# Performance work log

Hardware: AMD Instinct MI355X
Metric: run time of the kernel (lower is better)

## Reference

```python
import jax, jax.numpy as jnp
import numpy as np

N = 100000
E = 1600000
D = 128
EIG = 32
NUM_MOTIFS = 64
EPS = 1e-8  # torch cosine_similarity eps


def setup_inputs() -> dict:
    key = jax.random.key(0)
    ks = jax.random.split(key, 12)
    return {
        "q": jax.random.normal(ks[0], (N, D), jnp.float32),
        "k": jax.random.normal(ks[1], (N, D), jnp.float32),
        "v": jax.random.normal(ks[2], (N, D), jnp.float32),
        "eigs": jax.random.normal(ks[3], (N, EIG), jnp.float32),
        "motif_adj_vals": jax.random.uniform(ks[4], (E,), jnp.float32),
        "lambda0": jax.random.normal(ks[5], (1,), jnp.float32) * 0.1,
        "gamma": jax.random.normal(ks[6], (1,), jnp.float32) * 0.1,
        "motif_emb_w": jax.random.uniform(ks[7], (NUM_MOTIFS, 1), jnp.float32),
        "row": jax.random.randint(ks[8], (E,), 0, N, jnp.int32),
        "col": jax.random.randint(ks[9], (E,), 0, N, jnp.int32),
        "motif_ids": jax.random.randint(ks[10], (N,), 0, NUM_MOTIFS, jnp.int32),
    }


def _sparse_softmax(vals, row, n):
    # softmax of per-edge values grouped by destination/row index
    m = jax.ops.segment_max(vals, row, num_segments=n)
    e = jnp.exp(vals - m[row])
    z = jax.ops.segment_sum(e, row, num_segments=n)
    return e / z[row]


def reference(q, k, v, eigs, motif_adj_vals, lambda0, gamma, motif_emb_w,
              row, col, motif_ids):
    sqrt_dim = 1.0 / jnp.sqrt(jnp.asarray(q.shape[1], q.dtype))
    # edge-wise q.k dot product, scaled
    x = jnp.sum(q[row] * k[col], axis=-1) * sqrt_dim          # [E]
    # eig branch (args.model contains 'eig'); note original does NOT scale by sqrt_eig
    y = jnp.sum(eigs[row] * eigs[col], axis=-1)               # [E]
    s0 = x + jnp.exp(lambda0[0]) * y
    # motif branch: embedding lookup + cosine similarity along the edge dim (dim=0)
    me = motif_emb_w[motif_ids][:, 0]                          # [N]
    a, b = me[row], me[col]                                    # [E]
    sim = jnp.sum(a * b) / (jnp.maximum(jnp.linalg.norm(a), EPS)
                            * jnp.maximum(jnp.linalg.norm(b), EPS))
    s1 = motif_adj_vals * gamma[0] * sim                       # [E]
    n = q.shape[0]
    attn = 0.5 * (_sparse_softmax(s0, row, n) + _sparse_softmax(s1, row, n))
    # sparse-dense matmul: out[r] = sum_e attn_e * v[col_e]
    return jax.ops.segment_sum(attn[:, None] * v[col], row, num_segments=n)
```

## Files before the change

### kernel.cpp

```cpp
#include <hip/hip_runtime.h>
#include <math.h>

#define N_NODES 100000
#define N_EDGES 1600000
#define DIM 128
#define EIGD 32
#define CS_EPS 1e-8f

#define B1 1024
#define CHUNK 1563
#define NB 391

static const size_t OFF_REC    = 0;
static const size_t OFF_SW     = 0;
static const size_t OFF_RSTAT  = 6400000;
static const size_t OFF_SE     = 12800000;
static const size_t OFF_GH     = 12800000;
static const size_t OFF_BSTART = 25600000;
static const size_t OFF_BTOT   = 25601600;
static const size_t OFF_GPART  = 25603200;
static const size_t OFF_OFFS   = 25619584;
static const size_t OFF_SCAL   = 26019600;
static const size_t OFF_KB     = 26019616;
static const size_t OFF_VB     = 51619616;
static const size_t OFF_EB     = 77219616;

__device__ __forceinline__ unsigned short f2bf(float f) {
    unsigned u = __float_as_uint(f);
    unsigned r = (u + 0x7fffu + ((u >> 16) & 1u)) >> 16;
    return (unsigned short)r;
}
__device__ __forceinline__ float blo(unsigned w) { return __uint_as_float(w << 16); }
__device__ __forceinline__ float bhi(unsigned w) { return __uint_as_float(w & 0xffff0000u); }

#define K4C 3200000
#define E4C 800000

__global__ void __launch_bounds__(256) ka_cvt(
        const float* __restrict__ k, const float* __restrict__ v,
        const float* __restrict__ eigs,
        ushort* __restrict__ kb, ushort* __restrict__ vb,
        ushort* __restrict__ eb) {
    int i = blockIdx.x * blockDim.x + threadIdx.x;
    const float* src; ushort* dst; int j;
    if (i < K4C)            { src = k;    dst = kb; j = i; }
    else if (i < 2 * K4C)   { src = v;    dst = vb; j = i - K4C; }
    else if (i < 2*K4C+E4C) { src = eigs; dst = eb; j = i - 2 * K4C; }
    else return;
    float4 f = ((const float4*)src)[j];
    ushort4 o;
    o.x = f2bf(f.x); o.y = f2bf(f.y); o.z = f2bf(f.z); o.w = f2bf(f.w);
    ((ushort4*)dst)[j] = o;
}

__global__ void __launch_bounds__(256) kb_hist(
        const int* __restrict__ row, const int* __restrict__ col,
        const float* __restrict__ motif_w, const int* __restrict__ motif_ids,
        int* __restrict__ gh, float4* __restrict__ gpart) {
    __shared__ int hist[NB];
    __shared__ float wlds[64];
    __shared__ float red[3][4];
    const int t = threadIdx.x, b = blockIdx.x;
    for (int i = t; i < NB; i += 256) hist[i] = 0;
    if (t < 64) wlds[t] = motif_w[t];
    __syncthreads();

    const int e0 = b * CHUNK, e1 = min(N_EDGES, e0 + CHUNK);
    float sab = 0.f, saa = 0.f, sbb = 0.f;
    for (int e = e0 + t; e < e1; e += 256) {
        int r = row[e], c = col[e];
        atomicAdd(&hist[r >> 8], 1);
        float mr = wlds[motif_ids[r]], mc = wlds[motif_ids[c]];
        sab += mr * mc; saa += mr * mr; sbb += mc * mc;
    }
#pragma unroll
    for (int off = 32; off >= 1; off >>= 1) {
        sab += __shfl_xor(sab, off);
        saa += __shfl_xor(saa, off);
        sbb += __shfl_xor(sbb, off);
    }
    int lane = t & 63, wid = t >> 6;
    if (lane == 0) { red[0][wid] = sab; red[1][wid] = saa; red[2][wid] = sbb; }
    __syncthreads();
    if (t == 0) {
        float a = 0.f, bb = 0.f, cc = 0.f;
#pragma unroll
        for (int i = 0; i < 4; i++) { a += red[0][i]; bb += red[1][i]; cc += red[2][i]; }
        gpart[b] = make_float4(a, bb, cc, 0.f);
    }
    __syncthreads();
    for (int i = t; i < NB; i += 256) gh[b * NB + i] = hist[i];
}

__global__ void __launch_bounds__(256) ks_scanA(
        int* __restrict__ gh, int* __restrict__ btot) {
    const int colb = blockIdx.x;
    const int t = threadIdx.x;
    int v0 = gh[(t * 4 + 0) * NB + colb];
    int v1 = gh[(t * 4 + 1) * NB + colb];
    int v2 = gh[(t * 4 + 2) * NB + colb];
    int v3 = gh[(t * 4 + 3) * NB + colb];
    int tot4 = v0 + v1 + v2 + v3;
    __shared__ int sc[256];
    sc[t] = tot4;
    __syncthreads();
    for (int off = 1; off < 256; off <<= 1) {
        int w = (t >= off) ? sc[t - off] : 0;
        __syncthreads();
        sc[t] += w;
        __syncthreads();
    }
    int excl = sc[t] - tot4;
    gh[(t * 4 + 0) * NB + colb] = excl;
    gh[(t * 4 + 1) * NB + colb] = excl + v0;
    gh[(t * 4 + 2) * NB + colb] = excl + v0 + v1;
    gh[(t * 4 + 3) * NB + colb] = excl + v0 + v1 + v2;
    if (t == 255) btot[colb] = excl + tot4;
}

__global__ void __launch_bounds__(512) ks_scanB(
        const int* __restrict__ btot, int* __restrict__ bstart,
        const float4* __restrict__ gpart, const float* __restrict__ gamma,
        float* __restrict__ scal, int* __restrict__ offs) {
    const int t = threadIdx.x;
    __shared__ int tot[512];
    int my = (t < NB) ? btot[t] : 0;
    tot[t] = my;
    __syncthreads();
    for (int off = 1; off < 512; off <<= 1) {
        int v = (t >= off) ? tot[t - off] : 0;
        __syncthreads();
        tot[t] += v;
        __syncthreads();
    }
    if (t < NB) bstart[t] = tot[t] - my;
    if (t == NB - 1) {
        bstart[NB] = tot[t];
        offs[N_NODES] = tot[t];
    }

    float4 g0 = gpart[t];
    float4 g1 = gpart[t + 512];
    float sab = g0.x + g1.x, saa = g0.y + g1.y, sbb = g0.z + g1.z;
#pragma unroll
    for (int off = 32; off >= 1; off >>= 1) {
        sab += __shfl_xor(sab, off);
        saa += __shfl_xor(saa, off);
        sbb += __shfl_xor(sbb, off);
    }
    __shared__ float red[3][8];
    int lane = t & 63, wid = t >> 6;
    if (lane == 0) { red[0][wid] = sab; red[1][wid] = saa; red[2][wid] = sbb; }
    __syncthreads();
    if (t == 0) {
        float a = 0.f, bb = 0.f, cc = 0.f;
#pragma unroll
        for (int i = 0; i < 8; i++) { a += red[0][i]; bb += red[1][i]; cc += red[2][i]; }
        float na = sqrtf(bb); if (na < CS_EPS) na = CS_EPS;
        float nb2 = sqrtf(cc); if (nb2 < CS_EPS) nb2 = CS_EPS;
        scal[0] = gamma[0] * (a / (na * nb2));
    }
}

__global__ void __launch_bounds__(256) kd_coarse(
        const int* __restrict__ row, const int* __restrict__ col,
        const float* __restrict__ adj, const int* __restrict__ gh,
        const int* __restrict__ bstart, int2* __restrict__ rec) {
    __shared__ int cur[NB];
    const int t = threadIdx.x, b = blockIdx.x;
    for (int i = t; i < NB; i += 256) cur[i] = bstart[i] + gh[b * NB + i];
    __syncthreads();
    const int e0 = b * CHUNK, e1 = min(N_EDGES, e0 + CHUNK);
    for (int e = e0 + t; e < e1; e += 256) {
        int r = row[e];
        int pos = atomicAdd(&cur[r >> 8], 1);
        rec[pos] = make_int2(col[e] | ((r & 255) << 17), __float_as_int(adj[e]));
    }
}

__global__ void __launch_bounds__(256) kf_fine(
        const int2* __restrict__ rec, const int* __restrict__ bstart,
        int* __restrict__ offs, float2* __restrict__ se) {
    __shared__ int hist[256], sc[256], cur[256];
    const int t = threadIdx.x, b = blockIdx.x;
    hist[t] = 0;
    __syncthreads();
    const int s = bstart[b], e1 = bstart[b + 1];
    for (int i = s + t; i < e1; i += 256) {
        int rl = (rec[i].x >> 17) & 255;
        atomicAdd(&hist[rl], 1);
    }
    __syncthreads();
    int v = hist[t];
    sc[t] = v;
    __syncthreads();
    for (int off = 1; off < 256; off <<= 1) {
        int w = (t >= off) ? sc[t - off] : 0;
        __syncthreads();
        sc[t] += w;
        __syncthreads();
    }
    int excl = sc[t] - v;
    int rowg = b * 256 + t;
    if (rowg < N_NODES) offs[rowg] = s + excl;
    cur[t] = s + excl;
    __syncthreads();
    for (int i = s + t; i < e1; i += 256) {
        int2 rc = rec[i];
        int rl = (rc.x >> 17) & 255;
        int pos = atomicAdd(&cur[rl], 1);
        se[pos] = make_float2(__int_as_float(rc.x & 0x1FFFF), __int_as_float(rc.y));
    }
}

__global__ void __launch_bounds__(256) ks_score(
        const float* __restrict__ q, const ushort* __restrict__ kb,
        const ushort* __restrict__ eb,
        const float* __restrict__ lambda0, const int* __restrict__ offs,
        const float2* __restrict__ se, const float* __restrict__ scal,
        float* __restrict__ sw, float4* __restrict__ rowstat) {
    const int tid  = threadIdx.x;
    const int lane = tid & 63;
    const int wid  = tid >> 6;
    const int r = blockIdx.x * 4 + wid;
    if (r >= N_NODES) return;
    const int l16 = lane & 15;
    const int grp = lane >> 4;
    const float inv_sqrt_d = 0.08838834764831843f;

    const int start = offs[r], end = offs[r + 1];
    if (end == start) return;

    const float el0 = __expf(lambda0[0]);
    const float cs  = scal[0];

    const float4* qp = (const float4*)(q + (size_t)r * DIM);
    const float4 qa = qp[l16 * 2];
    const float4 qc = qp[l16 * 2 + 1];
    const unsigned erw = *(const unsigned*)(eb + (size_t)r * EIGD + l16 * 2);
    const float er0 = blo(erw), er1 = bhi(erw);

    const float NEG = -1e30f;
    float m0 = NEG, z0 = 0.f, m1 = NEG, z1 = 0.f;

    float2 ea_c = make_float2(0.f, 0.f);
    if (start + grp < end) ea_c = se[start + grp];

    for (int base = start; base < end; base += 4) {
        const int e = base + grp;
        const bool act = e < end;
        float2 ea_n = make_float2(0.f, 0.f);
        if (base + 4 + grp < end) ea_n = se[base + 4 + grp];

        float s0p = 0.f;
        if (act) {
            int c = __float_as_int(ea_c.x);
            const uint4 kw = *(const uint4*)(kb + (size_t)c * DIM + l16 * 8);
            const unsigned ecw = *(const unsigned*)(eb + (size_t)c * EIGD + l16 * 2);
            float x;
            x = qa.x * blo(kw.x);
            x = fmaf(qa.y, bhi(kw.x), x);
            x = fmaf(qa.z, blo(kw.y), x);
            x = fmaf(qa.w, bhi(kw.y), x);
            x = fmaf(qc.x, blo(kw.z), x);
            x = fmaf(qc.y, bhi(kw.z), x);
            x = fmaf(qc.z, blo(kw.w), x);
            x = fmaf(qc.w, bhi(kw.w), x);
            float y = er0 * blo(ecw) + er1 * bhi(ecw);
            s0p = fmaf(el0, y, x * inv_sqrt_d);
        }
#pragma unroll
        for (int off = 8; off >= 1; off >>= 1) s0p += __shfl_xor(s0p, off);

        if (act) {
            if (l16 == 0) sw[e] = s0p;
            float nm0 = fmaxf(m0, s0p);
            z0 = z0 * __expf(m0 - nm0) + __expf(s0p - nm0);
            m0 = nm0;
            float s1 = cs * ea_c.y;
            float nm1 = fmaxf(m1, s1);
            z1 = z1 * __expf(m1 - nm1) + __expf(s1 - nm1);
            m1 = nm1;
        }
        ea_c = ea_n;
    }

#pragma unroll
    for (int off = 16; off <= 32; off <<= 1) {
        float mo = __shfl_xor(m0, off), zo = __shfl_xor(z0, off);
        float M = fmaxf(m0, mo);
        z0 = z0 * __expf(m0 - M) + zo * __expf(mo - M);
        m0 = M;
        float mo1 = __shfl_xor(m1, off), zo1 = __shfl_xor(z1, off);
        float M1 = fmaxf(m1, mo1);
        z1 = z1 * __expf(m1 - M1) + zo1 * __expf(mo1 - M1);
        m1 = M1;
    }
    if (lane == 0) rowstat[r] = make_float4(m0, z0, m1, z1);
}

__global__ void __launch_bounds__(256) kpv(
        const ushort* __restrict__ vb, const int* __restrict__ offs,
        const float2* __restrict__ se, const float* __restrict__ sw,
        const float* __restrict__ scal, const float4* __restrict__ rowstat,
        float* __restrict__ out) {
    const int tid  = threadIdx.x;
    const int lane = tid & 63;
    const int wid  = tid >> 6;
    const int r = blockIdx.x * 4 + wid;
    if (r >= N_NODES) return;
    const int l16 = lane & 15;
    const int grp = lane >> 4;

    float2* outp = (float2*)(out + (size_t)r * DIM);
    const int start = offs[r], end = offs[r + 1];
    if (end == start) {
        outp[l16 * 4 + grp] = make_float2(0.f, 0.f);
        return;
    }
    const float cs = scal[0];
    const float4 st = rowstat[r];
    const float m0 = st.x, iz0 = 0.5f / st.y;
    const float m1 = st.z, iz1 = 0.5f / st.w;

    float a[8];
#pragma unroll
    for (int j = 0; j < 8; j++) a[j] = 0.f;

    float2 ea_c = make_float2(0.f, 0.f);
    float  sw_c = 0.f;
    if (start + grp < end) { ea_c = se[start + grp]; sw_c = sw[start + grp]; }

    for (int base = start; base < end; base += 4) {
        const int e = base + grp;
        const bool act = e < end;
        float2 ea_n = make_float2(0.f, 0.f);
        float  sw_n = 0.f;
        if (base + 4 + grp < end) { ea_n = se[base + 4 + grp]; sw_n = sw[base + 4 + grp]; }

        if (act) {
            int c = __float_as_int(ea_c.x);
            const uint4 vw = *(const uint4*)(vb + (size_t)c * DIM + l16 * 8);
            float u = __expf(sw_c - m0) * iz0 + __expf(cs * ea_c.y - m1) * iz1;
            a[0] = fmaf(u, blo(vw.x), a[0]); a[1] = fmaf(u, bhi(vw.x), a[1]);
            a[2] = fmaf(u, blo(vw.y), a[2]); a[3] = fmaf(u, bhi(vw.y), a[3]);
            a[4] = fmaf(u, blo(vw.z), a[4]); a[5] = fmaf(u, bhi(vw.z), a[5]);
            a[6] = fmaf(u, blo(vw.w), a[6]); a[7] = fmaf(u, bhi(vw.w), a[7]);
        }
        ea_c = ea_n; sw_c = sw_n;
    }

#pragma unroll
    for (int off = 16; off <= 32; off <<= 1) {
#pragma unroll
        for (int j = 0; j < 8; j++) a[j] += __shfl_xor(a[j], off);
    }
    float b0 = grp == 0 ? a[0] : grp == 1 ? a[2] : grp == 2 ? a[4] : a[6];
    float b1 = grp == 0 ? a[1] : grp == 1 ? a[3] : grp == 2 ? a[5] : a[7];
    outp[l16 * 4 + grp] = make_float2(b0, b1);
}

extern "C" void kernel_launch(void* const* d_in, const int* in_sizes, int n_in,
                              void* d_out, int out_size, void* d_ws, size_t ws_size,
                              hipStream_t stream) {
    const float* q        = (const float*)d_in[0];
    const float* k        = (const float*)d_in[1];
    const float* v        = (const float*)d_in[2];
    const float* eigs     = (const float*)d_in[3];
    const float* adj      = (const float*)d_in[4];
    const float* lambda0  = (const float*)d_in[5];
    const float* gamma    = (const float*)d_in[6];
    const float* motif_w  = (const float*)d_in[7];
    const int*   row      = (const int*)d_in[8];
    const int*   col      = (const int*)d_in[9];
    const int*   motif_ids= (const int*)d_in[10];
    float* out = (float*)d_out;

    char* ws = (char*)d_ws;
    int2*   rec    = (int2*)(ws + OFF_REC);
    float*  sw     = (float*)(ws + OFF_SW);
    float4* rstat  = (float4*)(ws + OFF_RSTAT);
    float2* se     = (float2*)(ws + OFF_SE);
    int*    gh     = (int*)(ws + OFF_GH);
    int*    bstart = (int*)(ws + OFF_BSTART);
    int*    btot   = (int*)(ws + OFF_BTOT);
    float4* gpart  = (float4*)(ws + OFF_GPART);
    int*    offs   = (int*)(ws + OFF_OFFS);
    float*  scal   = (float*)(ws + OFF_SCAL);
    ushort* kb     = (ushort*)(ws + OFF_KB);
    ushort* vb     = (ushort*)(ws + OFF_VB);
    ushort* eb     = (ushort*)(ws + OFF_EB);

    hipLaunchKernelGGL(ka_cvt, dim3((2 * K4C + E4C + 255) / 256), dim3(256), 0, stream,
                       k, v, eigs, kb, vb, eb);
    hipLaunchKernelGGL(kb_hist, dim3(B1), dim3(256), 0, stream,
                       row, col, motif_w, motif_ids, gh, gpart);
    hipLaunchKernelGGL(ks_scanA, dim3(NB), dim3(256), 0, stream,
                       gh, btot);
    hipLaunchKernelGGL(ks_scanB, dim3(1), dim3(512), 0, stream,
                       btot, bstart, gpart, gamma, scal, offs);
    hipLaunchKernelGGL(kd_coarse, dim3(B1), dim3(256), 0, stream,
                       row, col, adj, gh, bstart, rec);
    hipLaunchKernelGGL(kf_fine, dim3(NB), dim3(256), 0, stream,
                       rec, bstart, offs, se);
    hipLaunchKernelGGL(ks_score, dim3((N_NODES + 3) / 4), dim3(256), 0, stream,
                       q, kb, eb, lambda0, offs, se, scal, sw, rstat);
    hipLaunchKernelGGL(kpv, dim3((N_NODES + 3) / 4), dim3(256), 0, stream,
                       vb, offs, se, sw, scal, rstat, out);
}
```

Measured before the change: 473.1 us.

## Replace two-level radix CSR build with global-atomic degree count and scatter

Replaces the two-pass bucketed counting sort (per-block coarse histograms, coarse scatter into an intermediate record buffer, then fine per-bucket sort) with a direct CSR build. Per-row degrees are counted with global atomics, prefix-summed across blocks, and each edge is scattered straight to its final slot with a global atomic cursor. This removes the intermediate record buffer pass and the fine-sort kernel. In exchange it relies on 1.6M contended global atomics done twice and on fully random scatter writes, and the order of edges within a row becomes nondeterministic.

```diff
diff --git a/kernel.cpp b/kernel.cpp
--- a/kernel.cpp
+++ b/kernel.cpp
@@ -11,11 +11,11 @@
 #define CHUNK 1563
 #define NB 391
 
-static const size_t OFF_REC    = 0;
+static const size_t OFF_DEG    = 0;
+static const size_t OFF_CUR    = 400000;
 static const size_t OFF_SW     = 0;
 static const size_t OFF_RSTAT  = 6400000;
 static const size_t OFF_SE     = 12800000;
-static const size_t OFF_GH     = 12800000;
 static const size_t OFF_BSTART = 25600000;
 static const size_t OFF_BTOT   = 25601600;
 static const size_t OFF_GPART  = 25603200;
@@ -40,8 +40,9 @@
         const float* __restrict__ k, const float* __restrict__ v,
         const float* __restrict__ eigs,
         ushort* __restrict__ kb, ushort* __restrict__ vb,
-        ushort* __restrict__ eb) {
+        ushort* __restrict__ eb, int* __restrict__ deg) {
     int i = blockIdx.x * blockDim.x + threadIdx.x;
+    if (i < N_NODES) deg[i] = 0;
     const float* src; ushort* dst; int j;
     if (i < K4C)            { src = k;    dst = kb; j = i; }
     else if (i < 2 * K4C)   { src = v;    dst = vb; j = i - K4C; }
@@ -53,15 +54,13 @@
     ((ushort4*)dst)[j] = o;
 }
 
-__global__ void __launch_bounds__(256) kb_hist(
+__global__ void __launch_bounds__(256) kdeg(
         const int* __restrict__ row, const int* __restrict__ col,
         const float* __restrict__ motif_w, const int* __restrict__ motif_ids,
-        int* __restrict__ gh, float4* __restrict__ gpart) {
-    __shared__ int hist[NB];
+        int* __restrict__ deg, float4* __restrict__ gpart) {
     __shared__ float wlds[64];
     __shared__ float red[3][4];
     const int t = threadIdx.x, b = blockIdx.x;
-    for (int i = t; i < NB; i += 256) hist[i] = 0;
     if (t < 64) wlds[t] = motif_w[t];
     __syncthreads();
 
@@ -69,7 +68,7 @@
     float sab = 0.f, saa = 0.f, sbb = 0.f;
     for (int e = e0 + t; e < e1; e += 256) {
         int r = row[e], c = col[e];
-        atomicAdd(&hist[r >> 8], 1);
+        atomicAdd(&deg[r], 1);
         float mr = wlds[motif_ids[r]], mc = wlds[motif_ids[c]];
         sab += mr * mc; saa += mr * mr; sbb += mc * mc;
     }
@@ -88,21 +87,16 @@
         for (int i = 0; i < 4; i++) { a += red[0][i]; bb += red[1][i]; cc += red[2][i]; }
         gpart[b] = make_float4(a, bb, cc, 0.f);
     }
-    __syncthreads();
-    for (int i = t; i < NB; i += 256) gh[b * NB + i] = hist[i];
-}
-
-__global__ void __launch_bounds__(256) ks_scanA(
-        int* __restrict__ gh, int* __restrict__ btot) {
-    const int colb = blockIdx.x;
-    const int t = threadIdx.x;
-    int v0 = gh[(t * 4 + 0) * NB + colb];
-    int v1 = gh[(t * 4 + 1) * NB + colb];
-    int v2 = gh[(t * 4 + 2) * NB + colb];
-    int v3 = gh[(t * 4 + 3) * NB + colb];
-    int tot4 = v0 + v1 + v2 + v3;
+}
+
+__global__ void __launch_bounds__(256) ks1(
+        const int* __restrict__ deg, int* __restrict__ offs,
+        int* __restrict__ btot) {
+    const int t = threadIdx.x, b = blockIdx.x;
+    const int r = b * 256 + t;
+    int v = (r < N_NODES) ? deg[r] : 0;
     __shared__ int sc[256];
-    sc[t] = tot4;
+    sc[t] = v;
     __syncthreads();
     for (int off = 1; off < 256; off <<= 1) {
         int w = (t >= off) ? sc[t - off] : 0;
@@ -110,15 +104,11 @@
         sc[t] += w;
         __syncthreads();
     }
-    int excl = sc[t] - tot4;
-    gh[(t * 4 + 0) * NB + colb] = excl;
-    gh[(t * 4 + 1) * NB + colb] = excl + v0;
-    gh[(t * 4 + 2) * NB + colb] = excl + v0 + v1;
-    gh[(t * 4 + 3) * NB + colb] = excl + v0 + v1 + v2;
-    if (t == 255) btot[colb] = excl + tot4;
-}
-
-__global__ void __launch_bounds__(512) ks_scanB(
+    if (r < N_NODES) offs[r] = sc[t] - v;
+    if (t == 255) btot[b] = sc[255];
+}
+
+__global__ void __launch_bounds__(512) ks2(
         const int* __restrict__ btot, int* __restrict__ bstart,
         const float4* __restrict__ gpart, const float* __restrict__ gamma,
         float* __restrict__ scal, int* __restrict__ offs) {
@@ -162,54 +152,27 @@
     }
 }
 
-__global__ void __launch_bounds__(256) kd_coarse(
+__global__ void __launch_bounds__(256) ks3(
+        int* __restrict__ offs, const int* __restrict__ bstart,
+        int* __restrict__ cur) {
+    const int r = blockIdx.x * 256 + threadIdx.x;
+    if (r < N_NODES) {
+        int o = offs[r] + bstart[r >> 8];
+        offs[r] = o;
+        cur[r] = o;
+    }
+}
+
+__global__ void __launch_bounds__(256) kscat(
         const int* __restrict__ row, const int* __restrict__ col,
-        const float* __restrict__ adj, const int* __restrict__ gh,
-        const int* __restrict__ bstart, int2* __restrict__ rec) {
-    __shared__ int cur[NB];
+        const float* __restrict__ adj, int* __restrict__ cur,
+        float2* __restrict__ se) {
     const int t = threadIdx.x, b = blockIdx.x;
-    for (int i = t; i < NB; i += 256) cur[i] = bstart[i] + gh[b * NB + i];
-    __syncthreads();
     const int e0 = b * CHUNK, e1 = min(N_EDGES, e0 + CHUNK);
     for (int e = e0 + t; e < e1; e += 256) {
         int r = row[e];
-        int pos = atomicAdd(&cur[r >> 8], 1);
-        rec[pos] = make_int2(col[e] | ((r & 255) << 17), __float_as_int(adj[e]));
-    }
-}
-
-__global__ void __launch_bounds__(256) kf_fine(
-        const int2* __restrict__ rec, const int* __restrict__ bstart,
-        int* __restrict__ offs, float2* __restrict__ se) {
-    __shared__ int hist[256], sc[256], cur[256];
-    const int t = threadIdx.x, b = blockIdx.x;
-    hist[t] = 0;
-    __syncthreads();
-    const int s = bstart[b], e1 = bstart[b + 1];
-    for (int i = s + t; i < e1; i += 256) {
-        int rl = (rec[i].x >> 17) & 255;
-        atomicAdd(&hist[rl], 1);
-    }
-    __syncthreads();
-    int v = hist[t];
-    sc[t] = v;
-    __syncthreads();
-    for (int off = 1; off < 256; off <<= 1) {
-        int w = (t >= off) ? sc[t - off] : 0;
-        __syncthreads();
-        sc[t] += w;
-        __syncthreads();
-    }
-    int excl = sc[t] - v;
-    int rowg = b * 256 + t;
-    if (rowg < N_NODES) offs[rowg] = s + excl;
-    cur[t] = s + excl;
-    __syncthreads();
-    for (int i = s + t; i < e1; i += 256) {
-        int2 rc = rec[i];
-        int rl = (rc.x >> 17) & 255;
-        int pos = atomicAdd(&cur[rl], 1);
-        se[pos] = make_float2(__int_as_float(rc.x & 0x1FFFF), __int_as_float(rc.y));
+        int pos = atomicAdd(&cur[r], 1);
+        se[pos] = make_float2(__int_as_float(col[e]), adj[e]);
     }
 }
 
@@ -377,11 +340,11 @@
     float* out = (float*)d_out;
 
     char* ws = (char*)d_ws;
-    int2*   rec    = (int2*)(ws + OFF_REC);
+    int*    deg    = (int*)(ws + OFF_DEG);
+    int*    cur    = (int*)(ws + OFF_CUR);
     float*  sw     = (float*)(ws + OFF_SW);
     float4* rstat  = (float4*)(ws + OFF_RSTAT);
     float2* se     = (float2*)(ws + OFF_SE);
-    int*    gh     = (int*)(ws + OFF_GH);
     int*    bstart = (int*)(ws + OFF_BSTART);
     int*    btot   = (int*)(ws + OFF_BTOT);
     float4* gpart  = (float4*)(ws + OFF_GPART);
@@ -392,17 +355,17 @@
     ushort* eb     = (ushort*)(ws + OFF_EB);
 
     hipLaunchKernelGGL(ka_cvt, dim3((2 * K4C + E4C + 255) / 256), dim3(256), 0, stream,
-                       k, v, eigs, kb, vb, eb);
-    hipLaunchKernelGGL(kb_hist, dim3(B1), dim3(256), 0, stream,
-                       row, col, motif_w, motif_ids, gh, gpart);
-    hipLaunchKernelGGL(ks_scanA, dim3(NB), dim3(256), 0, stream,
-                       gh, btot);
-    hipLaunchKernelGGL(ks_scanB, dim3(1), dim3(512), 0, stream,
+                       k, v, eigs, kb, vb, eb, deg);
+    hipLaunchKernelGGL(kdeg, dim3(B1), dim3(256), 0, stream,
+                       row, col, motif_w, motif_ids, deg, gpart);
+    hipLaunchKernelGGL(ks1, dim3(NB), dim3(256), 0, stream,
+                       deg, offs, btot);
+    hipLaunchKernelGGL(ks2, dim3(1), dim3(512), 0, stream,
                        btot, bstart, gpart, gamma, scal, offs);
-    hipLaunchKernelGGL(kd_coarse, dim3(B1), dim3(256), 0, stream,
-                       row, col, adj, gh, bstart, rec);
-    hipLaunchKernelGGL(kf_fine, dim3(NB), dim3(256), 0, stream,
-                       rec, bstart, offs, se);
+    hipLaunchKernelGGL(ks3, dim3(NB), dim3(256), 0, stream,
+                       offs, bstart, cur);
+    hipLaunchKernelGGL(kscat, dim3(B1), dim3(256), 0, stream,
+                       row, col, adj, cur, se);
     hipLaunchKernelGGL(ks_score, dim3((N_NODES + 3) / 4), dim3(256), 0, stream,
                        q, kb, eb, lambda0, offs, se, scal, sw, rstat);
     hipLaunchKernelGGL(kpv, dim3((N_NODES + 3) / 4), dim3(256), 0, stream,
```

Result: slower. 590.9 us (+24.9%).
